# Performance work log

Hardware: AMD Instinct MI355X
Metric: run time of the kernel (lower is better)

Reference implementation:

```python
import jax, jax.numpy as jnp
import numpy as np

B, T, D, NH, V, L = 2, 1024, 1024, 16, 32000, 4  # L = blocks * layers_per_block
HD = D // NH
FF = 4 * D


def rmsnorm(x, gamma, beta):
    # matches RMSNorm: mean of squares over last dim (tp pmean is identity on 1 device)
    ms = jnp.mean(jnp.square(x), axis=-1, keepdims=True)
    return (x / jnp.sqrt(ms + 1e-6)) * gamma + beta


def setup_inputs() -> dict:
    key = jax.random.key(0)
    ks = jax.random.split(key, 16)
    s = 0.02
    inp = {
        "tokens": jax.random.randint(ks[0], (B, T), 0, V, dtype=jnp.int32),
        "emb_W": jax.random.normal(ks[1], (V, D), jnp.float32) * s,
        "pos_W": jax.random.normal(ks[2], (T, D), jnp.float32) * s,
        "g1": jnp.ones((L, D), jnp.float32),
        "be1": jnp.zeros((L, D), jnp.float32),
        "Wqkv": jax.random.normal(ks[3], (L, D, 3 * D), jnp.float32) * s,
        "bqkv": jnp.zeros((L, 3 * D), jnp.float32),
        "Wo": jax.random.normal(ks[4], (L, D, D), jnp.float32) * s,
        "bo": jnp.zeros((L, D), jnp.float32),
        "g2": jnp.ones((L, D), jnp.float32),
        "be2": jnp.zeros((L, D), jnp.float32),
        "Wf1": jax.random.normal(ks[5], (L, D, FF), jnp.float32) * s,
        "bf1": jnp.zeros((L, FF), jnp.float32),
        "Wf2": jax.random.normal(ks[6], (L, FF, D), jnp.float32) * s,
        "bf2": jnp.zeros((L, D), jnp.float32),
        "gf": jnp.ones((D,), jnp.float32),
        "bef": jnp.zeros((D,), jnp.float32),
    }
    return inp


def _forward(tokens, emb_W, pos_W, g1, be1, Wqkv, bqkv, Wo, bo, g2, be2,
             Wf1, bf1, Wf2, bf2, gf, bef):
    x = emb_W[tokens] + pos_W[jnp.arange(T)]  # [B, T, D]
    causal = jnp.tril(jnp.ones((T, T), dtype=bool))
    scale = HD ** -0.5
    for i in range(L):
        # attention sub-block
        h = rmsnorm(x, g1[i], be1[i])
        qkv = h @ Wqkv[i] + bqkv[i]
        q, k, v = jnp.split(qkv, 3, axis=-1)
        q = q.reshape(B, T, NH, HD).transpose(0, 2, 1, 3)  # B nh T d
        k = k.reshape(B, T, NH, HD).transpose(0, 2, 1, 3)
        v = v.reshape(B, T, NH, HD).transpose(0, 2, 1, 3)
        att = jnp.einsum('bhqd,bhkd->bhqk', q, k) * scale
        att = jnp.where(causal, att, -jnp.inf)
        att = jax.nn.softmax(att, axis=-1)
        o = jnp.einsum('bhqk,bhkd->bhqd', att, v)
        o = o.transpose(0, 2, 1, 3).reshape(B, T, D)
        x = x + (o @ Wo[i] + bo[i])
        # FFN sub-block (selu, dropout off since train=False)
        h = rmsnorm(x, g2[i], be2[i])
        f = jax.nn.selu(h @ Wf1[i] + bf1[i]) @ Wf2[i] + bf2[i]
        x = x + f
    # tied output head: final RMSNorm then embedding.attend
    x = rmsnorm(x, gf, bef)
    logits = jnp.einsum('btd,vd->btv', x, emb_W)
    return logits


def reference(tokens, emb_W, pos_W, g1, be1, Wqkv, bqkv, Wo, bo, g2, be2,
              Wf1, bf1, Wf2, bf2, gf, bef):
    return _forward(tokens, emb_W, pos_W, g1, be1, Wqkv, bqkv, Wo, bo,
                    g2, be2, Wf1, bf1, Wf2, bf2, gf, bef)
```

## Files before the change

kernel.cpp:

```cpp
#include <hip/hip_runtime.h>

typedef unsigned short u16;
typedef __attribute__((ext_vector_type(8))) short bf16x8;
typedef __attribute__((ext_vector_type(4))) float f32x4;

#define DD 1024
#define TT 1024
#define NHH 16
#define VV 32000
#define FFF 4096
#define LL 4
#define MM 2048
#define TD3 3072

__device__ __forceinline__ u16 f2bfu(float f) {
  unsigned int x = __builtin_bit_cast(unsigned int, f);
  return (u16)((x + 0x7FFFu + ((x >> 16) & 1u)) >> 16);
}

__device__ __forceinline__ void gl16(const u16* g, u16* l) {
  __builtin_amdgcn_global_load_lds((const __attribute__((address_space(1))) void*)g,
                                   (__attribute__((address_space(3))) void*)l, 16, 0, 0);
}

template <int N>
__device__ __forceinline__ void vwait() {
  if constexpr (N == 0) asm volatile("s_waitcnt vmcnt(0)" ::: "memory");
  else if constexpr (N == 4) asm volatile("s_waitcnt vmcnt(4)" ::: "memory");
  else asm volatile("s_waitcnt vmcnt(8)" ::: "memory");
}

__global__ void transpose_cvt_k(const float* __restrict__ in, u16* __restrict__ out,
                                int K, int N) {
  const size_t mat = (size_t)K * N;
  in += (size_t)blockIdx.z * mat;
  out += (size_t)blockIdx.z * mat;
  __shared__ float tile[32][33];
  const int n0 = blockIdx.x << 5, k0 = blockIdx.y << 5;
  const int tx = threadIdx.x, ty = threadIdx.y;
#pragma unroll
  for (int i = 0; i < 32; i += 8) tile[ty + i][tx] = in[(size_t)(k0 + ty + i) * N + n0 + tx];
  __syncthreads();
#pragma unroll
  for (int i = 0; i < 32; i += 8)
    out[(size_t)(n0 + ty + i) * K + k0 + tx] = f2bfu(tile[tx][ty + i]);
}

__global__ void cvt_bf16_k(const float* __restrict__ in, u16* __restrict__ out, long n4) {
  const long i = (long)blockIdx.x * blockDim.x + threadIdx.x;
  if (i >= n4) return;
  const float4 v = ((const float4*)in)[i];
  ushort4 o;
  o.x = f2bfu(v.x); o.y = f2bfu(v.y); o.z = f2bfu(v.z); o.w = f2bfu(v.w);
  ((ushort4*)out)[i] = o;
}

__global__ void embed_k(const int* __restrict__ tok, const float* __restrict__ emb,
                        const float* __restrict__ pos, float* __restrict__ x) {
  const int m = blockIdx.x, tid = threadIdx.x;
  const int t = m & (TT - 1);
  const int id = tok[m];
  const float4 e = ((const float4*)(emb + (size_t)id * DD))[tid];
  const float4 p = ((const float4*)(pos + (size_t)t * DD))[tid];
  float4 r;
  r.x = e.x + p.x; r.y = e.y + p.y; r.z = e.z + p.z; r.w = e.w + p.w;
  ((float4*)(x + (size_t)m * DD))[tid] = r;
}

__global__ void rmsnorm_k(const float* __restrict__ x, const float* __restrict__ g,
                          const float* __restrict__ be, u16* __restrict__ out) {
  const int row = blockIdx.x, tid = threadIdx.x;
  const float4 xv = ((const float4*)(x + (size_t)row * DD))[tid];
  float ss = xv.x * xv.x + xv.y * xv.y + xv.z * xv.z + xv.w * xv.w;
#pragma unroll
  for (int o = 32; o; o >>= 1) ss += __shfl_xor(ss, o);
  __shared__ float sm[4];
  if ((tid & 63) == 0) sm[tid >> 6] = ss;
  __syncthreads();
  const float tot = sm[0] + sm[1] + sm[2] + sm[3];
  const float rs = rsqrtf(tot * (1.f / DD) + 1e-6f);
  const float4 gv = ((const float4*)g)[tid];
  const float4 bv = ((const float4*)be)[tid];
  ushort4 o4;
  o4.x = f2bfu(xv.x * rs * gv.x + bv.x);
  o4.y = f2bfu(xv.y * rs * gv.y + bv.y);
  o4.z = f2bfu(xv.z * rs * gv.z + bv.z);
  o4.w = f2bfu(xv.w * rs * gv.w + bv.w);
  ((ushort4*)(out + (size_t)row * DD))[tid] = o4;
}

template <int NP>
__global__ void addres_rms_k(float* __restrict__ x, const float* __restrict__ pp,
                             const float* __restrict__ bias, const float* __restrict__ g,
                             const float* __restrict__ be, u16* __restrict__ out) {
  const int row = blockIdx.x, tid = threadIdx.x;
  const size_t base = (size_t)row * (DD / 4) + tid;
  float4 s = ((float4*)x)[base];
  const float4 bv = ((const float4*)bias)[tid];
  s.x += bv.x; s.y += bv.y; s.z += bv.z; s.w += bv.w;
#pragma unroll
  for (int p = 0; p < NP; ++p) {
    const float4 pv = ((const float4*)pp)[(size_t)p * (MM * DD / 4) + base];
    s.x += pv.x; s.y += pv.y; s.z += pv.z; s.w += pv.w;
  }
  ((float4*)x)[base] = s;
  float ss = s.x * s.x + s.y * s.y + s.z * s.z + s.w * s.w;
#pragma unroll
  for (int o = 32; o; o >>= 1) ss += __shfl_xor(ss, o);
  __shared__ float sm[4];
  if ((tid & 63) == 0) sm[tid >> 6] = ss;
  __syncthreads();
  const float tot = sm[0] + sm[1] + sm[2] + sm[3];
  const float rs = rsqrtf(tot * (1.f / DD) + 1e-6f);
  const float4 gv = ((const float4*)g)[tid];
  const float4 bev = ((const float4*)be)[tid];
  ushort4 o4;
  o4.x = f2bfu(s.x * rs * gv.x + bev.x);
  o4.y = f2bfu(s.y * rs * gv.y + bev.y);
  o4.z = f2bfu(s.z * rs * gv.z + bev.z);
  o4.w = f2bfu(s.w * rs * gv.w + bev.w);
  ((ushort4*)(out + (size_t)row * DD))[tid] = o4;
}

__global__ void pack_vt_k(const u16* __restrict__ qkv, u16* __restrict__ Vt) {
  const int z = blockIdx.x;
  const int t0 = blockIdx.y << 6;
  const int b = z >> 4, h = z & 15;
  __shared__ u16 tile[64][72];
  const int tid = threadIdx.x;
  for (int c = tid; c < 512; c += 256) {
    const int t = c >> 3, d8 = (c & 7) << 3;
    union { uint4 u; u16 s[8]; } tmp;
    tmp.u = *(const uint4*)(qkv + (long)(b * TT + t0 + t) * TD3 + 2 * DD + h * 64 + d8);
#pragma unroll
    for (int j = 0; j < 8; ++j) tile[d8 + j][t] = tmp.s[j];
  }
  __syncthreads();
  for (int c = tid; c < 512; c += 256) {
    const int d = c >> 3, t8 = (c & 7) << 3;
    *(uint4*)(Vt + ((long)z * 64 + d) * TT + t0 + t8) = *(const uint4*)&tile[d][t8];
  }
}

__global__ __launch_bounds__(256) void flash_k(const u16* __restrict__ qkv,
                                               const u16* __restrict__ Vt,
                                               u16* __restrict__ o) {
  const int z = blockIdx.x;
  const int pair = blockIdx.y;
  const int b = z >> 4, h = z & 15;
  const int tid = threadIdx.x;
  const int lane = tid & 63;
  const int w = tid >> 6;

  __shared__ u16 Qs[64 * 64];
  __shared__ u16 Ks[128 * 64];
  __shared__ u16 Vs[64 * 128];
  __shared__ u16 Ps[64 * 128];

  const u16* qbase = qkv + (size_t)b * TT * TD3;
  const int kcb = (lane >> 4) << 4;

  for (int half = 0; half < 2; ++half) {
    const int qa = half ? (15 - pair) : pair;
    const int q0 = qa << 6;
    const int nkt = (qa >> 1) + 1;

#pragma unroll
    for (int c = 0; c < 2; ++c) {
      const int rbase = c * 32 + w * 8;
      const int row = rbase + (lane >> 3);
      const u16* src = qbase + (long)(q0 + row) * TD3 + h * 64 +
                       ((((lane & 7) << 4) ^ ((row & 7) << 4)) >> 1);
      gl16(src, &Qs[rbase * 64]);
    }

    float m_r[4], l_r[4];
    f32x4 oacc[4];
#pragma unroll
    for (int r = 0; r < 4; ++r) { m_r[r] = -1e30f; l_r[r] = 0.f; }
#pragma unroll
    for (int nd = 0; nd < 4; ++nd) oacc[nd] = (f32x4){0.f, 0.f, 0.f, 0.f};

    for (int kt = 0; kt < nkt; ++kt) {
      const int t0 = kt << 7;
#pragma unroll
      for (int c = 0; c < 4; ++c) {
        const int rbase = c * 32 + w * 8;
        const int row = rbase + (lane >> 3);
        const u16* src = qbase + (long)(t0 + row) * TD3 + DD + h * 64 +
                         ((((lane & 7) << 4) ^ ((row & 7) << 4)) >> 1);
        gl16(src, &Ks[rbase * 64]);
      }
#pragma unroll
      for (int c = 0; c < 4; ++c) {
        const int rbase = c * 16 + w * 4;
        const int d = rbase + (lane >> 4);
        const u16* src = Vt + ((long)(z * 64 + d)) * TT + t0 +
                         ((((lane & 15) << 4) ^ ((d & 7) << 4)) >> 1);
        gl16(src, &Vs[rbase * 128]);
      }
      __syncthreads();

      f32x4 sacc[8];
#pragma unroll
      for (int ni = 0; ni < 8; ++ni) sacc[ni] = (f32x4){0.f, 0.f, 0.f, 0.f};
      const int qrow = (w << 4) + (lane & 15);
#pragma unroll
      for (int ks = 0; ks < 2; ++ks) {
        const bf16x8 aq = *(const bf16x8*)&Qs[qrow * 64 + (((ks * 64 + kcb) ^ ((qrow & 7) << 4)) >> 1)];
#pragma unroll
        for (int ni = 0; ni < 8; ++ni) {
          const int key = (lane & 15) + (ni << 4);
          const bf16x8 bk = *(const bf16x8*)&Ks[key * 64 + (((ks * 64 + kcb) ^ ((key & 7) << 4)) >> 1)];
          sacc[ni] = __builtin_amdgcn_mfma_f32_16x16x32_bf16(aq, bk, sacc[ni], 0, 0, 0);
        }
      }

      float mx[4] = {-1e30f, -1e30f, -1e30f, -1e30f};
      const bool diag = (kt == nkt - 1);
#pragma unroll
      for (int ni = 0; ni < 8; ++ni)
#pragma unroll
        for (int r = 0; r < 4; ++r) {
          float v = sacc[ni][r] * 0.125f;
          if (diag) {
            const int key = t0 + (lane & 15) + (ni << 4);
            const int qq = q0 + (w << 4) + ((lane >> 4) << 2) + r;
            if (key > qq) v = -1e30f;
          }
          sacc[ni][r] = v;
          mx[r] = fmaxf(mx[r], v);
        }
#pragma unroll
      for (int st = 1; st < 16; st <<= 1)
#pragma unroll
        for (int r = 0; r < 4; ++r) mx[r] = fmaxf(mx[r], __shfl_xor(mx[r], st));
      float sc[4], sum[4];
#pragma unroll
      for (int r = 0; r < 4; ++r) {
        const float mn = fmaxf(m_r[r], mx[r]);
        sc[r] = __expf(m_r[r] - mn);
        m_r[r] = mn;
        sum[r] = 0.f;
      }
#pragma unroll
      for (int ni = 0; ni < 8; ++ni)
#pragma unroll
        for (int r = 0; r < 4; ++r) {
          const float e = __expf(sacc[ni][r] - m_r[r]);
          sum[r] += e;
          const int prow = (w << 4) + ((lane >> 4) << 2) + r;
          const int pcol = (lane & 15) + (ni << 4);
          Ps[prow * 128 + (((pcol << 1) ^ ((prow & 7) << 4)) >> 1)] = f2bfu(e);
        }
#pragma unroll
      for (int st = 1; st < 16; st <<= 1)
#pragma unroll
        for (int r = 0; r < 4; ++r) sum[r] += __shfl_xor(sum[r], st);
#pragma unroll
      for (int r = 0; r < 4; ++r) l_r[r] = l_r[r] * sc[r] + sum[r];
#pragma unroll
      for (int nd = 0; nd < 4; ++nd)
#pragma unroll
        for (int r = 0; r < 4; ++r) oacc[nd][r] *= sc[r];

#pragma unroll
      for (int ks2 = 0; ks2 < 4; ++ks2) {
        const int prow = (w << 4) + (lane & 15);
        const bf16x8 pa = *(const bf16x8*)&Ps[prow * 128 + (((ks2 * 64 + kcb) ^ ((prow & 7) << 4)) >> 1)];
#pragma unroll
        for (int nd = 0; nd < 4; ++nd) {
          const int dd2 = (lane & 15) + (nd << 4);
          const bf16x8 vb = *(const bf16x8*)&Vs[dd2 * 128 + (((ks2 * 64 + kcb) ^ ((dd2 & 7) << 4)) >> 1)];
          oacc[nd] = __builtin_amdgcn_mfma_f32_16x16x32_bf16(pa, vb, oacc[nd], 0, 0, 0);
        }
      }
      __syncthreads();
    }

    float inv[4];
#pragma unroll
    for (int r = 0; r < 4; ++r) inv[r] = 1.f / l_r[r];
#pragma unroll
    for (int nd = 0; nd < 4; ++nd)
#pragma unroll
      for (int r = 0; r < 4; ++r) {
        const int row = q0 + (w << 4) + ((lane >> 4) << 2) + r;
        const int col = (h << 6) + (lane & 15) + (nd << 4);
        o[(long)(b * TT + row) * DD + col] = f2bfu(oacc[nd][r] * inv[r]);
      }
  }
}

enum { EPI_BF16 = 0, EPI_BF16_BIAS = 1, EPI_SELU = 2, EPI_F32 = 3, EPI_RESID = 4 };

template <int EPI>
__global__ __launch_bounds__(256) void gemm_bt(
    const u16* __restrict__ A, long az1, long az2, int lda,
    const u16* __restrict__ Bt, long bz1, long bz2, int ldb,
    void* __restrict__ C, long cz1, long cz2, int ldc,
    const float* __restrict__ bias, int Nvalid, int K) {
  const int z = blockIdx.z;
  A += (long)(z >> 4) * az1 + (long)(z & 15) * az2;
  Bt += (long)(z >> 4) * bz1 + (long)(z & 15) * bz2;
  const long coff = (long)(z >> 4) * cz1 + (long)(z & 15) * cz2;

  __shared__ u16 ldsA[2][128 * 32];
  __shared__ u16 ldsB[2][128 * 32];

  const int tid = threadIdx.x;
  const int lane = tid & 63;
  const int wave = tid >> 6;
  const int wr = wave >> 1, wc = wave & 1;
  const int m0 = blockIdx.x << 7, n0 = blockIdx.y << 7;

  f32x4 acc[4][4];
#pragma unroll
  for (int i = 0; i < 4; ++i)
#pragma unroll
    for (int j = 0; j < 4; ++j) acc[i][j] = (f32x4){0.f, 0.f, 0.f, 0.f};

  auto STAGE = [&](int buf, int kt) {
    const int k0 = kt << 5;
#pragma unroll
    for (int p = 0; p < 2; ++p) {
      const int c = tid + (p << 8);
      const int row = c >> 2, col = (c & 3) << 3;
      gl16(A + (long)(m0 + row) * lda + k0 + col, &ldsA[buf][c << 3]);
      gl16(Bt + (long)(n0 + row) * ldb + k0 + col, &ldsB[buf][c << 3]);
    }
  };

  const int nk = K >> 5;
  STAGE(0, 0);
  __syncthreads();
  int cur = 0;
  for (int kt = 0; kt < nk; ++kt) {
    if (kt + 1 < nk) STAGE(cur ^ 1, kt + 1);
    const int rb = lane & 15;
    const int kc = (lane >> 4) << 3;
    bf16x8 af[4], bfr[4];
#pragma unroll
    for (int mi = 0; mi < 4; ++mi)
      af[mi] = *(const bf16x8*)&ldsA[cur][(((wr << 6) + (mi << 4) + rb) << 5) + kc];
#pragma unroll
    for (int ni = 0; ni < 4; ++ni)
      bfr[ni] = *(const bf16x8*)&ldsB[cur][(((wc << 6) + (ni << 4) + rb) << 5) + kc];
#pragma unroll
    for (int mi = 0; mi < 4; ++mi)
#pragma unroll
      for (int ni = 0; ni < 4; ++ni)
        acc[mi][ni] = __builtin_amdgcn_mfma_f32_16x16x32_bf16(af[mi], bfr[ni], acc[mi][ni], 0, 0, 0);
    __syncthreads();
    cur ^= 1;
  }

  const int row0 = m0 + (wr << 6) + ((lane >> 4) << 2);
  const int col0 = n0 + (wc << 6) + (lane & 15);
#pragma unroll
  for (int ni = 0; ni < 4; ++ni) {
    const int col = col0 + (ni << 4);
    if (col >= Nvalid) continue;
    float bv = 0.f;
    if (EPI == EPI_BF16_BIAS || EPI == EPI_SELU || EPI == EPI_RESID) bv = bias[col];
#pragma unroll
    for (int mi = 0; mi < 4; ++mi) {
#pragma unroll
      for (int r = 0; r < 4; ++r) {
        const int row = row0 + (mi << 4) + r;
        const long idx = coff + (long)row * ldc + col;
        float v = acc[mi][ni][r] + bv;
        if (EPI == EPI_SELU)
          v = v > 0.f ? 1.0507009873554805f * v : 1.7580993408473766f * (__expf(v) - 1.f);
        if (EPI == EPI_BF16 || EPI == EPI_BF16_BIAS || EPI == EPI_SELU)
          ((u16*)C)[idx] = f2bfu(v);
        else if (EPI == EPI_F32)
          ((float*)C)[idx] = v;
        else
          ((float*)C)[idx] += v;
      }
    }
  }
}

template <int EPI>
__global__ __launch_bounds__(256) void gemm_bt3(
    const u16* __restrict__ A, long az1, long az2, int lda,
    const u16* __restrict__ Bt, long bz1, long bz2, int ldb,
    void* __restrict__ C, long cz1, long cz2, int ldc,
    const float* __restrict__ bias, int Nvalid, int K) {
  const int z = blockIdx.z;
  A += (long)(z >> 4) * az1 + (long)(z & 15) * az2;
  Bt += (long)(z >> 4) * bz1 + (long)(z & 15) * bz2;
  const long coff = (long)(z >> 4) * cz1 + (long)(z & 15) * cz2;

  __shared__ u16 ldsA[3][128 * 32];
  __shared__ u16 ldsB[3][128 * 32];

  const int tid = threadIdx.x;
  const int lane = tid & 63;
  const int wave = tid >> 6;
  const int wr = wave >> 1, wc = wave & 1;
  const int m0 = blockIdx.x << 7, n0 = blockIdx.y << 7;

  f32x4 acc[4][4];
#pragma unroll
  for (int i = 0; i < 4; ++i)
#pragma unroll
    for (int j = 0; j < 4; ++j) acc[i][j] = (f32x4){0.f, 0.f, 0.f, 0.f};

  auto STAGE = [&](int buf, int kt) {
    const int k0 = kt << 5;
#pragma unroll
    for (int p = 0; p < 2; ++p) {
      const int c = tid + (p << 8);
      const int row = c >> 2, col = (c & 3) << 3;
      gl16(A + (long)(m0 + row) * lda + k0 + col, &ldsA[buf][c << 3]);
      gl16(Bt + (long)(n0 + row) * ldb + k0 + col, &ldsB[buf][c << 3]);
    }
  };

  const int nk = K >> 5;
  STAGE(0, 0);
  STAGE(1, 1);

  const int rb = lane & 15;
  const int kc = (lane >> 4) << 3;
  int cur = 0, stg = 2;
#pragma unroll 1
  for (int kt = 0; kt < nk; ++kt) {
    if (kt + 1 < nk) vwait<4>();
    else vwait<0>();
    __builtin_amdgcn_s_barrier();
    __builtin_amdgcn_sched_barrier(0);

    bf16x8 af[4], bfr[4];
#pragma unroll
    for (int mi = 0; mi < 4; ++mi)
      af[mi] = *(const bf16x8*)&ldsA[cur][(((wr << 6) + (mi << 4) + rb) << 5) + kc];
#pragma unroll
    for (int ni = 0; ni < 4; ++ni)
      bfr[ni] = *(const bf16x8*)&ldsB[cur][(((wc << 6) + (ni << 4) + rb) << 5) + kc];
    asm volatile("s_waitcnt lgkmcnt(0)" ::: "memory");
    __builtin_amdgcn_sched_barrier(0);
    __builtin_amdgcn_s_barrier();
    __builtin_amdgcn_sched_barrier(0);
    if (kt + 2 < nk) STAGE(stg, kt + 2);
    __builtin_amdgcn_sched_barrier(0);

    __builtin_amdgcn_s_setprio(1);
#pragma unroll
    for (int mi = 0; mi < 4; ++mi)
#pragma unroll
      for (int ni = 0; ni < 4; ++ni)
        acc[mi][ni] = __builtin_amdgcn_mfma_f32_16x16x32_bf16(af[mi], bfr[ni], acc[mi][ni], 0, 0, 0);
    __builtin_amdgcn_s_setprio(0);

    cur = (cur == 2) ? 0 : cur + 1;
    stg = (stg == 2) ? 0 : stg + 1;
  }

  const int row0 = m0 + (wr << 6) + ((lane >> 4) << 2);
  const int col0 = n0 + (wc << 6) + (lane & 15);
#pragma unroll
  for (int ni = 0; ni < 4; ++ni) {
    const int col = col0 + (ni << 4);
    if (col >= Nvalid) continue;
    float bv = 0.f;
    if (EPI == EPI_BF16_BIAS || EPI == EPI_SELU || EPI == EPI_RESID) bv = bias[col];
#pragma unroll
    for (int mi = 0; mi < 4; ++mi) {
#pragma unroll
      for (int r = 0; r < 4; ++r) {
        const int row = row0 + (mi << 4) + r;
        const long idx = coff + (long)row * ldc + col;
        float v = acc[mi][ni][r] + bv;
        if (EPI == EPI_SELU)
          v = v > 0.f ? 1.0507009873554805f * v : 1.7580993408473766f * (__expf(v) - 1.f);
        if (EPI == EPI_BF16 || EPI == EPI_BF16_BIAS || EPI == EPI_SELU)
          ((u16*)C)[idx] = f2bfu(v);
        else if (EPI == EPI_F32)
          ((float*)C)[idx] = v;
        else
          ((float*)C)[idx] += v;
      }
    }
  }
}

template <int EPI, int KDIM>
__global__ __launch_bounds__(512) void gemm256_k(
    const u16* __restrict__ A, int lda,
    const u16* __restrict__ Bt, int ldb,
    void* __restrict__ C, int ldc,
    const float* __restrict__ bias, int mm) {
  extern __shared__ u16 smem[];
  u16* SA = smem;
  u16* SB = smem + 24576;

  const int nwg = gridDim.x;
  const int q = nwg >> 3, r = nwg & 7;
  const int xcd = blockIdx.x & 7, loc = blockIdx.x >> 3;
  const int wg = (xcd < r) ? (xcd * (q + 1) + loc) : (r * (q + 1) + (xcd - r) * q + loc);
  const int m0 = (wg % mm) << 8;
  const int n0 = (wg / mm) << 8;

  const int tid = threadIdx.x;
  const int lane = tid & 63;
  const int w = tid >> 6;
  const int wr = w >> 2, wc = w & 3;
  const int l = lane & 15, kq = lane >> 4;

  f32x4 acc[8][4];
#pragma unroll
  for (int i = 0; i < 8; ++i)
#pragma unroll
    for (int j = 0; j < 4; ++j) acc[i][j] = (f32x4){0.f, 0.f, 0.f, 0.f};

  auto STAGE = [&](int p, int kt) {
    u16* la = SA + (p << 13);
    u16* lb = SB + (p << 13);
    const int k0 = kt << 5;
#pragma unroll
    for (int hh = 0; hh < 2; ++hh) {
      const int c = tid + (hh << 9);
      const int r2 = c >> 3, sp = c & 7;
      const int s = sp ^ (r2 & 7);
      const int row = r2 + ((s >> 2) << 7);
      const int col = k0 + ((s & 3) << 3);
      gl16(A + (size_t)(m0 + row) * lda + col, la + (c << 3));
      gl16(Bt + (size_t)(n0 + row) * ldb + col, lb + (c << 3));
    }
  };

  constexpr int NK = KDIM >> 5;
  STAGE(0, 0);
  STAGE(1, 1);
  STAGE(2, 2);

  int buf = 0;
#pragma unroll 1
  for (int t = 0; t < NK; ++t) {
    if (t + 2 < NK) vwait<8>();
    else if (t + 1 < NK) vwait<4>();
    else vwait<0>();
    __builtin_amdgcn_s_barrier();
    __builtin_amdgcn_sched_barrier(0);

    const u16* a = SA + (buf << 13);
    const u16* b = SB + (buf << 13);
    auto rdA = [&](int mi) -> bf16x8 {
      const int row = (wr << 7) + (mi << 4) + l;
      const int r2 = row & 127;
      const int sp = (((row >> 7) << 2) + kq) ^ (r2 & 7);
      return *(const bf16x8*)&a[(r2 << 6) + (sp << 3)];
    };
    auto rdB = [&](int ni) -> bf16x8 {
      const int row = (wc << 6) + (ni << 4) + l;
      const int r2 = row & 127;
      const int sp = (((row >> 7) << 2) + kq) ^ (r2 & 7);
      return *(const bf16x8*)&b[(r2 << 6) + (sp << 3)];
    };

    bf16x8 bfr[4], afA[2], afB[2];
    bfr[0] = rdB(0); bfr[1] = rdB(1); bfr[2] = rdB(2); bfr[3] = rdB(3);
    afA[0] = rdA(0); afA[1] = rdA(1);
    __builtin_amdgcn_sched_barrier(0);
    afB[0] = rdA(2); afB[1] = rdA(3);
    __builtin_amdgcn_sched_barrier(0);

    __builtin_amdgcn_s_setprio(1);
#pragma unroll
    for (int ni = 0; ni < 4; ++ni) {
      acc[0][ni] = __builtin_amdgcn_mfma_f32_16x16x32_bf16(afA[0], bfr[ni], acc[0][ni], 0, 0, 0);
      acc[1][ni] = __builtin_amdgcn_mfma_f32_16x16x32_bf16(afA[1], bfr[ni], acc[1][ni], 0, 0, 0);
    }
    __builtin_amdgcn_s_setprio(0);
    __builtin_amdgcn_sched_barrier(0);
    afA[0] = rdA(4); afA[1] = rdA(5);
    __builtin_amdgcn_sched_barrier(0);
    __builtin_amdgcn_s_setprio(1);
#pragma unroll
    for (int ni = 0; ni < 4; ++ni) {
      acc[2][ni] = __builtin_amdgcn_mfma_f32_16x16x32_bf16(afB[0], bfr[ni], acc[2][ni], 0, 0, 0);
      acc[3][ni] = __builtin_amdgcn_mfma_f32_16x16x32_bf16(afB[1], bfr[ni], acc[3][ni], 0, 0, 0);
    }
    __builtin_amdgcn_s_setprio(0);
    __builtin_amdgcn_sched_barrier(0);
    afB[0] = rdA(6); afB[1] = rdA(7);
    __builtin_amdgcn_sched_barrier(0);
    __builtin_amdgcn_s_setprio(1);
#pragma unroll
    for (int ni = 0; ni < 4; ++ni) {
      acc[4][ni] = __builtin_amdgcn_mfma_f32_16x16x32_bf16(afA[0], bfr[ni], acc[4][ni], 0, 0, 0);
      acc[5][ni] = __builtin_amdgcn_mfma_f32_16x16x32_bf16(afA[1], bfr[ni], acc[5][ni], 0, 0, 0);
    }
    __builtin_amdgcn_s_setprio(0);
    __builtin_amdgcn_sched_barrier(0);

    asm volatile("s_waitcnt lgkmcnt(0)" ::: "memory");
    __builtin_amdgcn_sched_barrier(0);
    __builtin_amdgcn_s_barrier();
    __builtin_amdgcn_sched_barrier(0);
    if (t + 3 < NK) STAGE(buf, t + 3);
    __builtin_amdgcn_sched_barrier(0);

    __builtin_amdgcn_s_setprio(1);
#pragma unroll
    for (int ni = 0; ni < 4; ++ni) {
      acc[6][ni] = __builtin_amdgcn_mfma_f32_16x16x32_bf16(afB[0], bfr[ni], acc[6][ni], 0, 0, 0);
      acc[7][ni] = __builtin_amdgcn_mfma_f32_16x16x32_bf16(afB[1], bfr[ni], acc[7][ni], 0, 0, 0);
    }
    __builtin_amdgcn_s_setprio(0);
    buf = (buf == 2) ? 0 : buf + 1;
  }

  const int row0 = m0 + (wr << 7) + ((lane >> 4) << 2);
  const int col0 = n0 + (wc << 6) + (lane & 15);
#pragma unroll
  for (int ni = 0; ni < 4; ++ni) {
    const int col = col0 + (ni << 4);
    float bv = 0.f;
    if (EPI == EPI_BF16_BIAS || EPI == EPI_SELU) bv = bias[col];
#pragma unroll
    for (int mi = 0; mi < 8; ++mi) {
#pragma unroll
      for (int r = 0; r < 4; ++r) {
        const int row = row0 + (mi << 4) + r;
        const long idx = (long)row * ldc + col;
        float v = acc[mi][ni][r] + bv;
        if (EPI == EPI_SELU)
          v = v > 0.f ? 1.0507009873554805f * v : 1.7580993408473766f * (__expf(v) - 1.f);
        if (EPI == EPI_BF16 || EPI == EPI_BF16_BIAS || EPI == EPI_SELU)
          ((u16*)C)[idx] = f2bfu(v);
        else
          ((float*)C)[idx] = v;
      }
    }
  }
}

extern "C" void kernel_launch(void* const* d_in, const int* in_sizes, int n_in,
                              void* d_out, int out_size, void* d_ws, size_t ws_size,
                              hipStream_t stream) {
  const int* tokens = (const int*)d_in[0];
  const float* emb_W = (const float*)d_in[1];
  const float* pos_W = (const float*)d_in[2];
  const float* g1 = (const float*)d_in[3];
  const float* be1 = (const float*)d_in[4];
  const float* Wqkv = (const float*)d_in[5];
  const float* bqkv = (const float*)d_in[6];
  const float* Wo = (const float*)d_in[7];
  const float* bo = (const float*)d_in[8];
  const float* g2 = (const float*)d_in[9];
  const float* be2 = (const float*)d_in[10];
  const float* Wf1 = (const float*)d_in[11];
  const float* bf1 = (const float*)d_in[12];
  const float* Wf2 = (const float*)d_in[13];
  const float* bf2 = (const float*)d_in[14];
  const float* gf = (const float*)d_in[15];
  const float* bef = (const float*)d_in[16];

  char* w = (char*)d_ws;
  auto alloc = [&](size_t bytes) {
    char* p = w;
    w += (bytes + 255) & ~(size_t)255;
    return p;
  };
  u16* WqkvT = (u16*)alloc((size_t)LL * TD3 * DD * 2);
  u16* WoT   = (u16*)alloc((size_t)LL * DD * DD * 2);
  u16* Wf1T  = (u16*)alloc((size_t)LL * FFF * DD * 2);
  u16* Wf2T  = (u16*)alloc((size_t)LL * DD * FFF * 2);
  u16* embB  = (u16*)alloc((size_t)VV * DD * 2);
  float* x   = (float*)alloc((size_t)MM * DD * 4);
  u16* h     = (u16*)alloc((size_t)MM * DD * 2);
  u16* qkv   = (u16*)alloc((size_t)MM * TD3 * 2);
  u16* Vt    = (u16*)alloc((size_t)32 * 64 * TT * 2);
  u16* o     = (u16*)alloc((size_t)MM * DD * 2);
  u16* h1    = (u16*)alloc((size_t)MM * FFF * 2);
  float* pp  = (float*)alloc((size_t)4 * MM * DD * 4);

  bool big =
      hipFuncSetAttribute((const void*)&gemm256_k<EPI_F32, 1024>,
                          hipFuncAttributeMaxDynamicSharedMemorySize, 98304) == hipSuccess;

  dim3 tb(32, 8);
  transpose_cvt_k<<<dim3(TD3 / 32, DD / 32, LL), tb, 0, stream>>>(Wqkv, WqkvT, DD, TD3);
  transpose_cvt_k<<<dim3(DD / 32, DD / 32, LL), tb, 0, stream>>>(Wo, WoT, DD, DD);
  transpose_cvt_k<<<dim3(FFF / 32, DD / 32, LL), tb, 0, stream>>>(Wf1, Wf1T, DD, FFF);
  transpose_cvt_k<<<dim3(DD / 32, FFF / 32, LL), tb, 0, stream>>>(Wf2, Wf2T, FFF, DD);
  cvt_bf16_k<<<(VV * DD / 4) / 256, 256, 0, stream>>>(emb_W, embB, (long)VV * DD / 4);
  embed_k<<<MM, 256, 0, stream>>>(tokens, emb_W, pos_W, x);
  rmsnorm_k<<<MM, 256, 0, stream>>>(x, g1, be1, h);

  for (int i = 0; i < LL; ++i) {
    gemm_bt3<EPI_BF16_BIAS><<<dim3(16, 24, 1), 256, 0, stream>>>(
        h, 0, 0, DD, WqkvT + (size_t)i * TD3 * DD, 0, 0, DD,
        qkv, 0, 0, TD3, bqkv + i * TD3, TD3, DD);
    pack_vt_k<<<dim3(32, 16), 256, 0, stream>>>(qkv, Vt);
    flash_k<<<dim3(32, 8), 256, 0, stream>>>(qkv, Vt, o);
    gemm_bt3<EPI_F32><<<dim3(16, 8, 2), 256, 0, stream>>>(
        o, 0, 512, DD, WoT + (size_t)i * DD * DD, 0, 512, DD,
        pp, 0, (long)MM * DD, DD, nullptr, DD, 512);
    addres_rms_k<2><<<MM, 256, 0, stream>>>(x, pp, bo + i * DD, g2 + i * DD, be2 + i * DD, h);
    gemm_bt3<EPI_SELU><<<dim3(16, 32, 1), 256, 0, stream>>>(
        h, 0, 0, DD, Wf1T + (size_t)i * FFF * DD, 0, 0, DD,
        h1, 0, 0, FFF, bf1 + i * FFF, FFF, DD);
    gemm_bt3<EPI_F32><<<dim3(16, 8, 4), 256, 0, stream>>>(
        h1, 0, 1024, FFF, Wf2T + (size_t)i * DD * FFF, 0, 1024, FFF,
        pp, 0, (long)MM * DD, DD, nullptr, DD, 1024);
    const bool last = (i == LL - 1);
    addres_rms_k<4><<<MM, 256, 0, stream>>>(
        x, pp, bf2 + i * DD,
        last ? gf : g1 + (i + 1) * DD, last ? bef : be1 + (i + 1) * DD, h);
  }

  if (big) {
    gemm256_k<EPI_F32, 1024><<<1000, 512, 98304, stream>>>(
        h, DD, embB, DD, (float*)d_out, VV, nullptr, 8);
  } else {
    gemm_bt<EPI_F32><<<dim3(16, 250, 1), 256, 0, stream>>>(
        h, 0, 0, DD, embB, 0, 0, DD,
        (float*)d_out, 0, 0, VV, nullptr, VV, DD);
  }
}
```

Baseline: 959.2 us.

## Switch vocab GEMM to double buffering and widen weight transpose stores

The 256x256 output-head GEMM moves from a three-stage LDS pipeline with interleaved fragment loads and MFMAs to a two-stage buffer. Each K step now loads all fragments, barriers, issues the next prefetch, then runs all 32 MFMAs. This cuts LDS use from 96KB to 64KB, which may allow more occupancy, but it gives up the deeper prefetch and the fine-grained overlap of LDS reads with math. Separately, the weight transpose/convert kernel now uses 64x32 tiles and writes 16-byte vectors per thread instead of scattered 2-byte stores.

```diff
diff --git a/kernel.cpp b/kernel.cpp
--- a/kernel.cpp
+++ b/kernel.cpp
@@ -35,15 +35,19 @@
   const size_t mat = (size_t)K * N;
   in += (size_t)blockIdx.z * mat;
   out += (size_t)blockIdx.z * mat;
-  __shared__ float tile[32][33];
-  const int n0 = blockIdx.x << 5, k0 = blockIdx.y << 5;
+  __shared__ float tile[32][65];
+  const int n0 = blockIdx.x << 6, k0 = blockIdx.y << 5;
   const int tx = threadIdx.x, ty = threadIdx.y;
 #pragma unroll
-  for (int i = 0; i < 32; i += 8) tile[ty + i][tx] = in[(size_t)(k0 + ty + i) * N + n0 + tx];
+  for (int i = 0; i < 8; ++i)
+    tile[(ty << 3) + i][tx] = in[(size_t)(k0 + (ty << 3) + i) * N + n0 + tx];
   __syncthreads();
-#pragma unroll
-  for (int i = 0; i < 32; i += 8)
-    out[(size_t)(n0 + ty + i) * K + k0 + tx] = f2bfu(tile[tx][ty + i]);
+  const int tid = (ty << 6) + tx;
+  const int n = tid >> 2, oct = (tid & 3) << 3;
+  union { u16 s[8]; uint4 u[1]; ulong2 v; } tmp;
+#pragma unroll
+  for (int j = 0; j < 8; ++j) tmp.s[j] = f2bfu(tile[oct + j][n]);
+  *(uint4*)(out + (size_t)(n0 + n) * K + k0 + oct) = tmp.u[0];
 }
 
 __global__ void cvt_bf16_k(const float* __restrict__ in, u16* __restrict__ out, long n4) {
@@ -496,7 +500,7 @@
     const float* __restrict__ bias, int mm) {
   extern __shared__ u16 smem[];
   u16* SA = smem;
-  u16* SB = smem + 24576;
+  u16* SB = smem + 16384;
 
   const int nwg = gridDim.x;
   const int q = nwg >> 3, r = nwg & 7;
@@ -536,13 +540,11 @@
   constexpr int NK = KDIM >> 5;
   STAGE(0, 0);
   STAGE(1, 1);
-  STAGE(2, 2);
 
   int buf = 0;
 #pragma unroll 1
   for (int t = 0; t < NK; ++t) {
-    if (t + 2 < NK) vwait<8>();
-    else if (t + 1 < NK) vwait<4>();
+    if (t + 1 < NK) vwait<4>();
     else vwait<0>();
     __builtin_amdgcn_s_barrier();
     __builtin_amdgcn_sched_barrier(0);
@@ -562,57 +564,26 @@
       return *(const bf16x8*)&b[(r2 << 6) + (sp << 3)];
     };
 
-    bf16x8 bfr[4], afA[2], afB[2];
-    bfr[0] = rdB(0); bfr[1] = rdB(1); bfr[2] = rdB(2); bfr[3] = rdB(3);
-    afA[0] = rdA(0); afA[1] = rdA(1);
-    __builtin_amdgcn_sched_barrier(0);
-    afB[0] = rdA(2); afB[1] = rdA(3);
+    bf16x8 af[8], bfr[4];
+#pragma unroll
+    for (int ni = 0; ni < 4; ++ni) bfr[ni] = rdB(ni);
+#pragma unroll
+    for (int mi = 0; mi < 8; ++mi) af[mi] = rdA(mi);
+    asm volatile("s_waitcnt lgkmcnt(0)" ::: "memory");
+    __builtin_amdgcn_sched_barrier(0);
+    __builtin_amdgcn_s_barrier();
+    __builtin_amdgcn_sched_barrier(0);
+    if (t + 2 < NK) STAGE(buf, t + 2);
     __builtin_amdgcn_sched_barrier(0);
 
     __builtin_amdgcn_s_setprio(1);
 #pragma unroll
-    for (int ni = 0; ni < 4; ++ni) {
-      acc[0][ni] = __builtin_amdgcn_mfma_f32_16x16x32_bf16(afA[0], bfr[ni], acc[0][ni], 0, 0, 0);
-      acc[1][ni] = __builtin_amdgcn_mfma_f32_16x16x32_bf16(afA[1], bfr[ni], acc[1][ni], 0, 0, 0);
-    }
+    for (int mi = 0; mi < 8; ++mi)
+#pragma unroll
+      for (int ni = 0; ni < 4; ++ni)
+        acc[mi][ni] = __builtin_amdgcn_mfma_f32_16x16x32_bf16(af[mi], bfr[ni], acc[mi][ni], 0, 0, 0);
     __builtin_amdgcn_s_setprio(0);
-    __builtin_amdgcn_sched_barrier(0);
-    afA[0] = rdA(4); afA[1] = rdA(5);
-    __builtin_amdgcn_sched_barrier(0);
-    __builtin_amdgcn_s_setprio(1);
-#pragma unroll
-    for (int ni = 0; ni < 4; ++ni) {
-      acc[2][ni] = __builtin_amdgcn_mfma_f32_16x16x32_bf16(afB[0], bfr[ni], acc[2][ni], 0, 0, 0);
-      acc[3][ni] = __builtin_amdgcn_mfma_f32_16x16x32_bf16(afB[1], bfr[ni], acc[3][ni], 0, 0, 0);
-    }
-    __builtin_amdgcn_s_setprio(0);
-    __builtin_amdgcn_sched_barrier(0);
-    afB[0] = rdA(6); afB[1] = rdA(7);
-    __builtin_amdgcn_sched_barrier(0);
-    __builtin_amdgcn_s_setprio(1);
-#pragma unroll
-    for (int ni = 0; ni < 4; ++ni) {
-      acc[4][ni] = __builtin_amdgcn_mfma_f32_16x16x32_bf16(afA[0], bfr[ni], acc[4][ni], 0, 0, 0);
-      acc[5][ni] = __builtin_amdgcn_mfma_f32_16x16x32_bf16(afA[1], bfr[ni], acc[5][ni], 0, 0, 0);
-    }
-    __builtin_amdgcn_s_setprio(0);
-    __builtin_amdgcn_sched_barrier(0);
-
-    asm volatile("s_waitcnt lgkmcnt(0)" ::: "memory");
-    __builtin_amdgcn_sched_barrier(0);
-    __builtin_amdgcn_s_barrier();
-    __builtin_amdgcn_sched_barrier(0);
-    if (t + 3 < NK) STAGE(buf, t + 3);
-    __builtin_amdgcn_sched_barrier(0);
-
-    __builtin_amdgcn_s_setprio(1);
-#pragma unroll
-    for (int ni = 0; ni < 4; ++ni) {
-      acc[6][ni] = __builtin_amdgcn_mfma_f32_16x16x32_bf16(afB[0], bfr[ni], acc[6][ni], 0, 0, 0);
-      acc[7][ni] = __builtin_amdgcn_mfma_f32_16x16x32_bf16(afB[1], bfr[ni], acc[7][ni], 0, 0, 0);
-    }
-    __builtin_amdgcn_s_setprio(0);
-    buf = (buf == 2) ? 0 : buf + 1;
+    buf ^= 1;
   }
 
   const int row0 = m0 + (wr << 7) + ((lane >> 4) << 2);
@@ -682,13 +653,13 @@
 
   bool big =
       hipFuncSetAttribute((const void*)&gemm256_k<EPI_F32, 1024>,
-                          hipFuncAttributeMaxDynamicSharedMemorySize, 98304) == hipSuccess;
-
-  dim3 tb(32, 8);
-  transpose_cvt_k<<<dim3(TD3 / 32, DD / 32, LL), tb, 0, stream>>>(Wqkv, WqkvT, DD, TD3);
-  transpose_cvt_k<<<dim3(DD / 32, DD / 32, LL), tb, 0, stream>>>(Wo, WoT, DD, DD);
-  transpose_cvt_k<<<dim3(FFF / 32, DD / 32, LL), tb, 0, stream>>>(Wf1, Wf1T, DD, FFF);
-  transpose_cvt_k<<<dim3(DD / 32, FFF / 32, LL), tb, 0, stream>>>(Wf2, Wf2T, FFF, DD);
+                          hipFuncAttributeMaxDynamicSharedMemorySize, 65536) == hipSuccess;
+
+  dim3 tb2(64, 4);
+  transpose_cvt_k<<<dim3(TD3 / 64, DD / 32, LL), tb2, 0, stream>>>(Wqkv, WqkvT, DD, TD3);
+  transpose_cvt_k<<<dim3(DD / 64, DD / 32, LL), tb2, 0, stream>>>(Wo, WoT, DD, DD);
+  transpose_cvt_k<<<dim3(FFF / 64, DD / 32, LL), tb2, 0, stream>>>(Wf1, Wf1T, DD, FFF);
+  transpose_cvt_k<<<dim3(DD / 64, FFF / 32, LL), tb2, 0, stream>>>(Wf2, Wf2T, FFF, DD);
   cvt_bf16_k<<<(VV * DD / 4) / 256, 256, 0, stream>>>(emb_W, embB, (long)VV * DD / 4);
   embed_k<<<MM, 256, 0, stream>>>(tokens, emb_W, pos_W, x);
   rmsnorm_k<<<MM, 256, 0, stream>>>(x, g1, be1, h);
@@ -716,7 +687,7 @@
   }
 
   if (big) {
-    gemm256_k<EPI_F32, 1024><<<1000, 512, 98304, stream>>>(
+    gemm256_k<EPI_F32, 1024><<<1000, 512, 65536, stream>>>(
         h, DD, embB, DD, (float*)d_out, VV, nullptr, 8);
   } else {
     gemm_bt<EPI_F32><<<dim3(16, 250, 1), 256, 0, stream>>>(
```

Result: no change. 960.7 us (+0.2%).
